# Kernel optimization log

Hardware: AMD Instinct MI355X
Metric: run time of the kernel (lower is better)

The kernel has to match this reference:

```python
import jax, jax.numpy as jnp
import numpy as np

N, E, D, ED, T, L = 10000, 160000, 128, 64, 4, 3
FIN, FOUT = D, D // T  # divide_input=False -> F_in = hidden; F_out = hidden // towers


def _w(key, *shape):
    return jax.random.normal(key, shape, dtype=jnp.float32) * 0.05


def setup_inputs() -> dict:
    key = jax.random.key(0)
    ks = iter(jax.random.split(key, 64))
    inp = {
        "x": jax.random.normal(next(ks), (N, D), jnp.float32),
        "edge_index": jax.random.randint(next(ks), (2, E), 0, N, jnp.int32),
        "edge_attr": jax.random.normal(next(ks), (E, ED), jnp.float32),
        # per-layer PNAConv params (stacked over L layers, T towers)
        "enc_W": _w(next(ks), L, ED, FIN), "enc_b": _w(next(ks), L, FIN),
        "pre_W1": _w(next(ks), L, T, 3 * FIN, FIN), "pre_b1": _w(next(ks), L, T, FIN),
        "pre_W2": _w(next(ks), L, T, FIN, FIN), "pre_b2": _w(next(ks), L, T, FIN),
        "post_W1": _w(next(ks), L, T, 4 * FIN, FOUT), "post_b1": _w(next(ks), L, T, FOUT),
        "post_W2": _w(next(ks), L, T, FOUT, FOUT), "post_b2": _w(next(ks), L, T, FOUT),
        "lin_W": _w(next(ks), L, D, D), "lin_b": _w(next(ks), L, D),
        # GRU (gate order r, z, n as in torch)
        "gru_Wi": _w(next(ks), D, 3 * D), "gru_Wh": _w(next(ks), D, 3 * D),
        "gru_bi": _w(next(ks), 3 * D), "gru_bh": _w(next(ks), 3 * D),
        # edge-update MLPs (shared across layers, as in the module)
        "fcu_W1": _w(next(ks), D, 2 * D), "fcu_b1": _w(next(ks), 2 * D),
        "fcu_W2": _w(next(ks), 2 * D, 2 * D), "fcu_b2": _w(next(ks), 2 * D),
        "fcv_W1": _w(next(ks), D, 2 * D), "fcv_b1": _w(next(ks), 2 * D),
        "fcv_W2": _w(next(ks), 2 * D, 2 * D), "fcv_b2": _w(next(ks), 2 * D),
        "fc_W1": _w(next(ks), 2 * D, 2 * D), "fc_b1": _w(next(ks), 2 * D),
        "fc_W2": _w(next(ks), 2 * D, ED), "fc_b2": _w(next(ks), ED),
        "eu_W1": _w(next(ks), 2 * ED, 2 * ED), "eu_b1": _w(next(ks), 2 * ED),
        "eu_W2": _w(next(ks), 2 * ED, ED), "eu_b2": _w(next(ks), ED),
    }
    return inp


def _pna_conv(x, src, dst, edge_attr, enc_W, enc_b, pW1, pb1, pW2, pb2,
              qW1, qb1, qW2, qb2, lW, lb):
    # message: pre-MLP on cat(x_i, x_j, enc(edge_attr)); split first Linear to avoid cat.
    e = edge_attr @ enc_W + enc_b                              # [E, FIN]
    Wi, Wj, We = pW1[:, :FIN], pW1[:, FIN:2 * FIN], pW1[:, 2 * FIN:]
    h = (jnp.einsum('ef,tfo->eto', x[dst], Wi)
         + jnp.einsum('ef,tfo->eto', x[src], Wj)
         + jnp.einsum('ef,tfo->eto', e, We) + pb1)             # [E, T, FIN]
    msg = jnp.einsum('etf,tfo->eto', jax.nn.relu(h), pW2) + pb2  # [E, T, FIN]
    # aggregate at target nodes (dst): mean / max / std
    cnt = jnp.maximum(jax.ops.segment_sum(jnp.ones((E,), msg.dtype), dst, N), 1.0)[:, None, None]
    mean = jax.ops.segment_sum(msg, dst, N) / cnt
    mean_sq = jax.ops.segment_sum(msg * msg, dst, N) / cnt
    std = jnp.sqrt(jax.nn.relu(mean_sq - mean * mean) + 1e-5)
    mx = jax.ops.segment_max(msg, dst, N)
    mx = jnp.where(jnp.isfinite(mx), mx, 0.0)
    xt = jnp.broadcast_to(x[:, None, :], (N, T, FIN))
    out = jnp.concatenate([xt, mean, mx, std], axis=-1)        # [N, T, 4*FIN]
    out = jax.nn.relu(jnp.einsum('ntf,tfo->nto', out, qW1) + qb1)
    out = jnp.einsum('ntf,tfo->nto', out, qW2) + qb2           # [N, T, FOUT]
    return out.reshape(N, D) @ lW + lb


def _gru(m, h, Wi, Wh, bi, bh):
    gi = m @ Wi + bi
    gh = h @ Wh + bh
    ir, iz, inn = jnp.split(gi, 3, axis=-1)
    hr, hz, hn = jnp.split(gh, 3, axis=-1)
    r = jax.nn.sigmoid(ir + hr)
    z = jax.nn.sigmoid(iz + hz)
    n = jnp.tanh(inn + r * hn)
    return (1.0 - z) * n + z * h


def _forward(x, edge_index, edge_attr,
             enc_W, enc_b, pre_W1, pre_b1, pre_W2, pre_b2,
             post_W1, post_b1, post_W2, post_b2, lin_W, lin_b,
             gru_Wi, gru_Wh, gru_bi, gru_bh,
             fcu_W1, fcu_b1, fcu_W2, fcu_b2,
             fcv_W1, fcv_b1, fcv_W2, fcv_b2,
             fc_W1, fc_b1, fc_W2, fc_b2,
             eu_W1, eu_b1, eu_W2, eu_b2):
    src, dst = edge_index[0], edge_index[1]
    out, h = x, x
    for i in range(L):
        m = _pna_conv(out, src, dst, edge_attr,
                      enc_W[i], enc_b[i], pre_W1[i], pre_b1[i], pre_W2[i], pre_b2[i],
                      post_W1[i], post_b1[i], post_W2[i], post_b2[i], lin_W[i], lin_b[i])
        h = _gru(m, h, gru_Wi, gru_Wh, gru_bi, gru_bh)
        out = h
        u, v = out[src], out[dst]
        fu = jax.nn.relu(jax.nn.relu(u @ fcu_W1 + fcu_b1) @ fcu_W2 + fcu_b2)
        fv = jax.nn.relu(jax.nn.relu(v @ fcv_W1 + fcv_b1) @ fcv_W2 + fcv_b2)
        m_ed = jax.nn.relu(jax.nn.relu(fu * fv @ fc_W1 + fc_b1) @ fc_W2 + fc_b2)
        edge_attr = jax.nn.relu(jnp.concatenate([m_ed, edge_attr], axis=1) @ eu_W1 + eu_b1) @ eu_W2 + eu_b2
    return out, edge_attr


def reference(x, edge_index, edge_attr,
              enc_W, enc_b, pre_W1, pre_b1, pre_W2, pre_b2,
              post_W1, post_b1, post_W2, post_b2, lin_W, lin_b,
              gru_Wi, gru_Wh, gru_bi, gru_bh,
              fcu_W1, fcu_b1, fcu_W2, fcu_b2,
              fcv_W1, fcv_b1, fcv_W2, fcv_b2,
              fc_W1, fc_b1, fc_W2, fc_b2,
              eu_W1, eu_b1, eu_W2, eu_b2):
    out, ea = _forward(x, edge_index, edge_attr,
                       enc_W, enc_b, pre_W1, pre_b1, pre_W2, pre_b2,
                       post_W1, post_b1, post_W2, post_b2, lin_W, lin_b,
                       gru_Wi, gru_Wh, gru_bi, gru_bh,
                       fcu_W1, fcu_b1, fcu_W2, fcu_b2,
                       fcv_W1, fcv_b1, fcv_W2, fcv_b2,
                       fc_W1, fc_b1, fc_W2, fc_b2,
                       eu_W1, eu_b1, eu_W2, eu_b2)
    return (out, ea, out)
```

## Files before the change

### kernel.cpp

```cpp
#include <hip/hip_runtime.h>
#include <hip/hip_bf16.h>
#include <math.h>

#define GN 10000
#define GNP 10112
#define GE 160000
#define GT 4
#define GL 3

typedef __attribute__((ext_vector_type(8))) short short8;
typedef __attribute__((ext_vector_type(4))) float f32x4;
typedef unsigned short u16;
typedef unsigned int u32;

__device__ __forceinline__ u16 f2b(float f) {
  unsigned u = __float_as_uint(f);
  unsigned r = (u + 0x7FFFu + ((u >> 16) & 1u)) >> 16;
  return (u16)r;
}
__device__ __forceinline__ float b2f(u16 b) {
  return __uint_as_float(((unsigned)b) << 16);
}

__device__ __forceinline__ void gl_lds16(const void* g, void* l) {
  __builtin_amdgcn_global_load_lds(
      (const __attribute__((address_space(1))) void*)g,
      (__attribute__((address_space(3))) void*)l, 16, 0, 0);
}

__device__ __forceinline__ int xcd_swz(int orig, int nwg) {
  int q = nwg >> 3, r = nwg & 7;
  int xcd = orig & 7, idx = orig >> 3;
  return (xcd < r ? xcd * (q + 1) : r * (q + 1) + (xcd - r) * q) + idx;
}

__global__ __launch_bounds__(256) void gemmz_k(
    const float* __restrict__ A0, const float* __restrict__ B0,
    const float* __restrict__ bias0, u16* __restrict__ Cv,
    int M, int N, int K, int lda, int ldb, int ldc,
    size_t aZ, size_t btZ, size_t bZ, int cCol)
{
  __shared__ float As[16][65];
  __shared__ float Bs[16][65];
  const int z = blockIdx.z;
  const float* A = A0 + (size_t)z * aZ;
  const float* B = B0 + (size_t)z * btZ;
  const float* bias = bias0 + (size_t)z * bZ;
  const int tid = threadIdx.x;
  const int brow = blockIdx.y * 64;
  const int tr = ((tid >> 4) & 15) << 2;
  const int tc = (tid & 15) << 2;
  float acc[4][4] = {{0.f}};

  for (int k0 = 0; k0 < K; k0 += 16) {
    for (int i = tid; i < 64 * 16; i += 256) {
      int r = i >> 4, c = i & 15;
      int gr = brow + r, gk = k0 + c;
      float v = 0.f;
      if (gr < M && gk < K) v = A[(size_t)gr * lda + gk];
      As[c][r] = v;
    }
    for (int i = tid; i < 16 * 64; i += 256) {
      int r = i >> 6, c = i & 63;
      int gk = k0 + r;
      Bs[r][c] = (gk < K && c < N) ? B[(size_t)gk * ldb + c] : 0.f;
    }
    __syncthreads();
#pragma unroll
    for (int kk = 0; kk < 16; ++kk) {
      float a[4], b[4];
#pragma unroll
      for (int i = 0; i < 4; ++i) a[i] = As[kk][tr + i];
#pragma unroll
      for (int j = 0; j < 4; ++j) b[j] = Bs[kk][tc + j];
#pragma unroll
      for (int i = 0; i < 4; ++i)
#pragma unroll
        for (int j = 0; j < 4; ++j) acc[i][j] += a[i] * b[j];
    }
    __syncthreads();
  }

#pragma unroll
  for (int i = 0; i < 4; ++i) {
    int gr = brow + tr + i;
    if (gr >= M) continue;
#pragma unroll
    for (int j = 0; j < 4; ++j) {
      int gc = tc + j;
      if (gc >= N) continue;
      Cv[(size_t)gr * ldc + z * cCol + gc] = f2b(acc[i][j] + bias[gc]);
    }
  }
}

template<bool RELU, bool OUTB, bool EAFILL>
__global__ __launch_bounds__(256) void mgemm_k(
    const u16* __restrict__ A,
    const u16* __restrict__ Bt, const float* __restrict__ bias,
    void* __restrict__ Cv,
    int M, int N, int K, int lda, int ldc,
    const float* __restrict__ ea, long e0)
{
  __shared__ u16 As[64 * 64];
  __shared__ u16 Bs[64 * 64];
  const int tid = threadIdx.x;
  const int brow = blockIdx.y * 64, bcol = blockIdx.x * 64;
  const int wid = tid >> 6, lane = tid & 63;
  const int wr = wid >> 1, wc = wid & 1;
  const int lrow = lane & 15, lk8 = (lane >> 4) * 8;

  f32x4 acc[2][2] = {};

  for (int k0 = 0; k0 < K; k0 += 64) {
#pragma unroll
    for (int s = 0; s < 2; ++s) {
      int c = tid + s * 256;
      int r = c >> 3, kq = (c & 7) * 8;
      const u16* sp = A + (size_t)(brow + r) * lda + k0 + kq;
      short8 v = *(const short8*)sp;
      int byt = (r * 128 + kq * 2) ^ ((r & 7) << 4);
      *(short8*)((char*)As + byt) = v;
    }
#pragma unroll
    for (int s = 0; s < 2; ++s) {
      int c = tid + s * 256;
      int r = c >> 3, kq = (c & 7) * 8;
      const u16* sp = Bt + (size_t)(bcol + r) * K + k0 + kq;
      short8 v = *(const short8*)sp;
      int byt = (r * 128 + kq * 2) ^ ((r & 7) << 4);
      *(short8*)((char*)Bs + byt) = v;
    }
    __syncthreads();
#pragma unroll
    for (int ks = 0; ks < 2; ++ks) {
      short8 a[2], b[2];
#pragma unroll
      for (int m = 0; m < 2; ++m) {
        int r = wr * 32 + m * 16 + lrow;
        int kk = ks * 32 + lk8;
        int byt = (r * 128 + kk * 2) ^ ((r & 7) << 4);
        a[m] = *(const short8*)((const char*)As + byt);
      }
#pragma unroll
      for (int n = 0; n < 2; ++n) {
        int r = wc * 32 + n * 16 + lrow;
        int kk = ks * 32 + lk8;
        int byt = (r * 128 + kk * 2) ^ ((r & 7) << 4);
        b[n] = *(const short8*)((const char*)Bs + byt);
      }
#pragma unroll
      for (int m = 0; m < 2; ++m)
#pragma unroll
        for (int n = 0; n < 2; ++n)
          acc[m][n] = __builtin_amdgcn_mfma_f32_16x16x32_bf16(a[m], b[n], acc[m][n], 0, 0, 0);
    }
    __syncthreads();
  }

#pragma unroll
  for (int m = 0; m < 2; ++m)
#pragma unroll
    for (int n = 0; n < 2; ++n) {
      int col = bcol + wc * 32 + n * 16 + (lane & 15);
      float bv = bias[col];
#pragma unroll
      for (int j = 0; j < 4; ++j) {
        int row = brow + wr * 32 + m * 16 + (lane >> 4) * 4 + j;
        float v = acc[m][n][j] + bv;
        if (RELU) v = fmaxf(v, 0.f);
        if (OUTB) ((u16*)Cv)[(size_t)row * ldc + col] = f2b(v);
        else      ((float*)Cv)[(size_t)row * ldc + col] = v;
      }
    }
  if (EAFILL) {
    for (int i = tid; i < 64 * 64; i += 256) {
      int r = i >> 6, c = i & 63;
      ((u16*)Cv)[(size_t)(brow + r) * 128 + 64 + c] =
          f2b(ea[(size_t)(e0 + brow + r) * 64 + c]);
    }
  }
}

template<bool RELU, bool OUTB>
__global__ __launch_bounds__(256) void mgemm_z_k(
    const u16* __restrict__ A0,
    const u16* __restrict__ Bt0, const float* __restrict__ bias0,
    void* __restrict__ Cv,
    int M, int N, int K, int lda, int ldc,
    size_t aZ, size_t btZ, size_t bZ, size_t cZ)
{
  __shared__ u16 As[64 * 64];
  __shared__ u16 Bs[64 * 64];
  const int z = blockIdx.z;
  const u16* A = A0 + (size_t)z * aZ;
  const u16* Bt = Bt0 + (size_t)z * btZ;
  const float* bias = bias0 + (size_t)z * bZ;
  const int tid = threadIdx.x;
  const int brow = blockIdx.y * 64, bcol = blockIdx.x * 64;
  const int wid = tid >> 6, lane = tid & 63;
  const int wr = wid >> 1, wc = wid & 1;
  const int lrow = lane & 15, lk8 = (lane >> 4) * 8;

  f32x4 acc[2][2] = {};

  for (int k0 = 0; k0 < K; k0 += 64) {
#pragma unroll
    for (int s = 0; s < 2; ++s) {
      int c = tid + s * 256;
      int r = c >> 3, kq = (c & 7) * 8;
      const u16* sp = A + (size_t)(brow + r) * lda + k0 + kq;
      short8 v = *(const short8*)sp;
      int byt = (r * 128 + kq * 2) ^ ((r & 7) << 4);
      *(short8*)((char*)As + byt) = v;
    }
#pragma unroll
    for (int s = 0; s < 2; ++s) {
      int c = tid + s * 256;
      int r = c >> 3, kq = (c & 7) * 8;
      const u16* sp = Bt + (size_t)(bcol + r) * K + k0 + kq;
      short8 v = *(const short8*)sp;
      int byt = (r * 128 + kq * 2) ^ ((r & 7) << 4);
      *(short8*)((char*)Bs + byt) = v;
    }
    __syncthreads();
#pragma unroll
    for (int ks = 0; ks < 2; ++ks) {
      short8 a[2], b[2];
#pragma unroll
      for (int m = 0; m < 2; ++m) {
        int r = wr * 32 + m * 16 + lrow;
        int kk = ks * 32 + lk8;
        int byt = (r * 128 + kk * 2) ^ ((r & 7) << 4);
        a[m] = *(const short8*)((const char*)As + byt);
      }
#pragma unroll
      for (int n = 0; n < 2; ++n) {
        int r = wc * 32 + n * 16 + lrow;
        int kk = ks * 32 + lk8;
        int byt = (r * 128 + kk * 2) ^ ((r & 7) << 4);
        b[n] = *(const short8*)((const char*)Bs + byt);
      }
#pragma unroll
      for (int m = 0; m < 2; ++m)
#pragma unroll
        for (int n = 0; n < 2; ++n)
          acc[m][n] = __builtin_amdgcn_mfma_f32_16x16x32_bf16(a[m], b[n], acc[m][n], 0, 0, 0);
    }
    __syncthreads();
  }

#pragma unroll
  for (int m = 0; m < 2; ++m)
#pragma unroll
    for (int n = 0; n < 2; ++n) {
      int col = bcol + wc * 32 + n * 16 + (lane & 15);
      float bv = bias[col];
#pragma unroll
      for (int j = 0; j < 4; ++j) {
        int row = brow + wr * 32 + m * 16 + (lane >> 4) * 4 + j;
        float v = acc[m][n][j] + bv;
        if (RELU) v = fmaxf(v, 0.f);
        if (OUTB) ((u16*)Cv + (size_t)z * cZ)[(size_t)row * ldc + col] = f2b(v);
        else      ((float*)Cv + (size_t)z * cZ)[(size_t)row * ldc + col] = v;
      }
    }
}

template<bool RELU, bool GATHER, bool MUL, bool OUTB>
__global__ __launch_bounds__(256) void mg2_k(
    const u16* __restrict__ A, const u16* __restrict__ A2,
    const int* __restrict__ idx, const int* __restrict__ idx2,
    const u16* __restrict__ Bt, const float* __restrict__ bias,
    void* __restrict__ Cv,
    int M, int N, int K, int lda, int ldc)
{
  __shared__ u16 As[128 * 64];
  __shared__ u16 Bs[128 * 64];
  __shared__ int ridx[128];
  __shared__ int ridx2[128];
  const int tid = threadIdx.x;
  const int brow = blockIdx.y * 128, bcol = blockIdx.x * 128;
  const int wid = tid >> 6, lane = tid & 63;
  const int wr = wid >> 1, wc = wid & 1;
  const int lrow = lane & 15, lkg = lane >> 4;

  if (GATHER) {
    if (tid < 128) {
      ridx[tid] = idx[brow + tid];
      if (MUL) ridx2[tid] = idx2[brow + tid];
    }
    __syncthreads();
  }

  f32x4 acc[4][4] = {};

  const char* srcA[4];
  const char* srcB[4];
#pragma unroll
  for (int s = 0; s < 4; ++s) {
    int i = tid + s * 256;
    int r = i >> 3, g = i & 7;
    size_t grow = GATHER ? (size_t)ridx[r] : (size_t)(brow + r);
    int gq = (g ^ (r & 7)) * 8;
    srcA[s] = (const char*)(A + grow * lda + gq);
    srcB[s] = (const char*)(Bt + (size_t)(bcol + r) * K + gq);
  }

  for (int k0 = 0; k0 < K; k0 += 64) {
    if constexpr (!MUL) {
#pragma unroll
      for (int s = 0; s < 4; ++s)
        gl_lds16(srcA[s] + (size_t)k0 * 2, (char*)As + s * 4096 + wid * 1024);
#pragma unroll
      for (int s = 0; s < 4; ++s)
        gl_lds16(srcB[s] + (size_t)k0 * 2, (char*)Bs + s * 4096 + wid * 1024);
    } else {
#pragma unroll
      for (int s = 0; s < 4; ++s) {
        int i = tid + s * 256;
        int r = i >> 3, kq = (i & 7) * 8;
        size_t grow = GATHER ? (size_t)ridx[r] : (size_t)(brow + r);
        size_t grow2 = GATHER ? (size_t)ridx2[r] : (size_t)(brow + r);
        const u16* sp = A + grow * lda + k0 + kq;
        short8 v = *(const short8*)sp;
        const u16* sp2 = A2 + grow2 * lda + k0 + kq;
        short8 v2 = *(const short8*)sp2;
#pragma unroll
        for (int e = 0; e < 8; ++e)
          v[e] = (short)f2b(b2f((u16)v[e]) * b2f((u16)v2[e]));
        int byt = (r * 128 + kq * 2) ^ ((r & 7) << 4);
        *(short8*)((char*)As + byt) = v;
      }
#pragma unroll
      for (int s = 0; s < 4; ++s) {
        int i = tid + s * 256;
        int r = i >> 3, kq = (i & 7) * 8;
        const u16* sp = Bt + (size_t)(bcol + r) * K + k0 + kq;
        short8 v = *(const short8*)sp;
        int byt = (r * 128 + kq * 2) ^ ((r & 7) << 4);
        *(short8*)((char*)Bs + byt) = v;
      }
    }
    __syncthreads();
#pragma unroll
    for (int ks = 0; ks < 2; ++ks) {
      const int kb = ks * 64 + lkg * 16;
      short8 a[4], b[4];
#pragma unroll
      for (int m = 0; m < 4; ++m) {
        int r = wr * 64 + m * 16 + lrow;
        int byt = (r * 128 + kb) ^ ((r & 7) << 4);
        a[m] = *(const short8*)((const char*)As + byt);
      }
#pragma unroll
      for (int n = 0; n < 4; ++n) {
        int r = wc * 64 + n * 16 + lrow;
        int byt = (r * 128 + kb) ^ ((r & 7) << 4);
        b[n] = *(const short8*)((const char*)Bs + byt);
      }
#pragma unroll
      for (int m = 0; m < 4; ++m)
#pragma unroll
        for (int n = 0; n < 4; ++n)
          acc[m][n] = __builtin_amdgcn_mfma_f32_16x16x32_bf16(a[m], b[n], acc[m][n], 0, 0, 0);
    }
    __syncthreads();
  }

#pragma unroll
  for (int m = 0; m < 4; ++m)
#pragma unroll
    for (int n = 0; n < 4; ++n) {
      int col = bcol + wc * 64 + n * 16 + lrow;
      float bv = bias[col];
#pragma unroll
      for (int j = 0; j < 4; ++j) {
        int row = brow + wr * 64 + m * 16 + lkg * 4 + j;
        float v = acc[m][n][j] + bv;
        if (RELU) v = fmaxf(v, 0.f);
        if (OUTB) ((u16*)Cv)[(size_t)row * ldc + col] = f2b(v);
        else      ((float*)Cv)[(size_t)row * ldc + col] = v;
      }
    }
}

__global__ __launch_bounds__(256) void convf_k(
    const u16* __restrict__ eab, const int* __restrict__ eidx,
    const int* __restrict__ src, const int* __restrict__ dst, long base,
    const u16* __restrict__ EWt, const float* __restrict__ bc,
    const u16* __restrict__ XIJ,
    const u16* __restrict__ W2t, const float* __restrict__ b2,
    float* __restrict__ sumb, float* __restrict__ sumsqb,
    unsigned* __restrict__ mxb, int Nn)
{
  __shared__ u16 AB[128 * 128];
  __shared__ u16 H[128 * 128];
  __shared__ int nid[128], sidm[128];
  u16* As = AB;
  u16* Bs = AB + 128 * 64;
  const int tid = threadIdx.x;
  const int brow = xcd_swz(blockIdx.x, gridDim.x) * 128;
  const int t = blockIdx.y;
  const int wid = tid >> 6, lane = tid & 63;
  const int wr = wid >> 1, wc = wid & 1;
  const int lrow = lane & 15, lkg = lane >> 4;

  __shared__ int eids[128];
  if (tid < 128) {
    int e = eidx[base + brow + tid];
    eids[tid] = e;
    nid[tid] = dst[e];
    sidm[tid] = src[e];
  }
  __syncthreads();

#pragma unroll
  for (int s = 0; s < 4; ++s) {
    int i = tid + s * 256;
    int r = i >> 3, g = i & 7;
    int gq = (g ^ (r & 7)) * 8;
    gl_lds16(eab + (size_t)eids[r] * 64 + gq, (char*)As + s * 4096 + wid * 1024);
  }
#pragma unroll
  for (int s = 0; s < 4; ++s) {
    int i = tid + s * 256;
    int r = i >> 3, g = i & 7;
    int gq = (g ^ (r & 7)) * 8;
    gl_lds16(EWt + (size_t)(t * 128 + r) * 64 + gq, (char*)Bs + s * 4096 + wid * 1024);
  }
  __syncthreads();

  f32x4 acc[4][4] = {};
#pragma unroll
  for (int ks = 0; ks < 2; ++ks) {
    const int kb = ks * 64 + lkg * 16;
    short8 a[4], b[4];
#pragma unroll
    for (int m = 0; m < 4; ++m) {
      int r = wr * 64 + m * 16 + lrow;
      int byt = (r * 128 + kb) ^ ((r & 7) << 4);
      a[m] = *(const short8*)((const char*)As + byt);
    }
#pragma unroll
    for (int n = 0; n < 4; ++n) {
      int r = wc * 64 + n * 16 + lrow;
      int byt = (r * 128 + kb) ^ ((r & 7) << 4);
      b[n] = *(const short8*)((const char*)Bs + byt);
    }
#pragma unroll
    for (int m = 0; m < 4; ++m)
#pragma unroll
      for (int n = 0; n < 4; ++n)
        acc[m][n] = __builtin_amdgcn_mfma_f32_16x16x32_bf16(a[m], b[n], acc[m][n], 0, 0, 0);
  }

#pragma unroll
  for (int m = 0; m < 4; ++m)
#pragma unroll
    for (int n = 0; n < 4; ++n) {
      int cl = wc * 64 + n * 16 + lrow;
      float bv = bc[t * 128 + cl];
#pragma unroll
      for (int j = 0; j < 4; ++j) {
        int rl = wr * 64 + m * 16 + lkg * 4 + j;
        int byt = (rl * 256 + cl * 2) ^ ((rl & 7) << 4);
        *(u16*)((char*)H + byt) = f2b(acc[m][n][j] + bv);
      }
    }
  __syncthreads();

#pragma unroll
  for (int s = 0; s < 8; ++s) {
    int i = tid + s * 256;
    int r = i >> 4, g = i & 15;
    int gs = (g & 8) | ((g & 7) ^ (r & 7));
    gl_lds16(W2t + (size_t)t * 16384 + (size_t)r * 128 + gs * 8,
             (char*)AB + s * 4096 + wid * 1024);
  }

#pragma unroll
  for (int s = 0; s < 8; ++s) {
    int i = tid + s * 256;
    int row = i >> 4, q = i & 15;
    int byt = (row * 256 + q * 16) ^ ((row & 7) << 4);
    short8 h8 = *(const short8*)((const char*)H + byt);
    short8 a8 = *(const short8*)(XIJ + (size_t)nid[row] * 1024 + t * 128 + q * 8);
    short8 c8 = *(const short8*)(XIJ + (size_t)sidm[row] * 1024 + 512 + t * 128 + q * 8);
#pragma unroll
    for (int e = 0; e < 8; ++e) {
      float v = b2f((u16)h8[e]) + b2f((u16)a8[e]) + b2f((u16)c8[e]);
      h8[e] = (short)f2b(fmaxf(v, 0.f));
    }
    *(short8*)((char*)H + byt) = h8;
  }
  __syncthreads();

  f32x4 acc2[4][4] = {};
#pragma unroll
  for (int ks = 0; ks < 4; ++ks) {
    const int kb = ks * 64 + lkg * 16;
    short8 a[4], b[4];
#pragma unroll
    for (int m = 0; m < 4; ++m) {
      int r = wr * 64 + m * 16 + lrow;
      int byt = (r * 256 + kb) ^ ((r & 7) << 4);
      a[m] = *(const short8*)((const char*)H + byt);
    }
#pragma unroll
    for (int n = 0; n < 4; ++n) {
      int c = wc * 64 + n * 16 + lrow;
      int byt = (c * 256 + kb) ^ ((c & 7) << 4);
      b[n] = *(const short8*)((const char*)AB + byt);
    }
#pragma unroll
    for (int m = 0; m < 4; ++m)
#pragma unroll
      for (int n = 0; n < 4; ++n)
        acc2[m][n] = __builtin_amdgcn_mfma_f32_16x16x32_bf16(a[m], b[n], acc2[m][n], 0, 0, 0);
  }
  __syncthreads();

#pragma unroll
  for (int m = 0; m < 4; ++m)
#pragma unroll
    for (int n = 0; n < 4; ++n) {
      int col = wc * 64 + n * 16 + lrow;
      float bv = b2[t * 128 + col];
#pragma unroll
      for (int j = 0; j < 4; ++j) {
        int row = wr * 64 + m * 16 + lkg * 4 + j;
        int byt = (row * 256 + col * 2) ^ ((row & 7) << 4);
        *(u16*)((char*)H + byt) = f2b(acc2[m][n][j] + bv);
      }
    }
  __syncthreads();

  {
    const int col = tid & 127, half = tid >> 7;
    const int r0 = half * 64;
    float* sb = sumb + (size_t)t * Nn * 128;
    float* qb = sumsqb + (size_t)t * Nn * 128;
    unsigned* xbp = mxb + (size_t)t * Nn * 128;
    int cur = nid[r0];
    float sacc = 0.f, qacc = 0.f, mxv = -INFINITY;
    for (int rr = 0; rr < 64; ++rr) {
      int row = r0 + rr;
      int nd = nid[row];
      if (nd != cur) {
        size_t o = (size_t)cur * 128 + col;
        atomicAdd(&sb[o], sacc);
        atomicAdd(&qb[o], qacc);
        unsigned ub = __float_as_uint(mxv);
        atomicMax(&xbp[o], (ub & 0x80000000u) ? ~ub : (ub | 0x80000000u));
        cur = nd; sacc = 0.f; qacc = 0.f; mxv = -INFINITY;
      }
      int byt = (row * 256 + col * 2) ^ ((row & 7) << 4);
      float v = b2f(*(const u16*)((const char*)H + byt));
      sacc += v; qacc += v * v; mxv = fmaxf(mxv, v);
    }
    size_t o = (size_t)cur * 128 + col;
    atomicAdd(&sb[o], sacc);
    atomicAdd(&qb[o], qacc);
    unsigned ub = __float_as_uint(mxv);
    atomicMax(&xbp[o], (ub & 0x80000000u) ? ~ub : (ub | 0x80000000u));
  }
}

__global__ __launch_bounds__(256) void eu_fused_k(
    const u16* __restrict__ C3b,
    const u16* __restrict__ euW1t, const float* __restrict__ eu_b1,
    const u16* __restrict__ euW2t, const float* __restrict__ eu_b2,
    float* __restrict__ EAp, u16* __restrict__ eab, long e0)
{
  __shared__ u16 SM[128 * 128];
  __shared__ u16 W2s[64 * 128];
  u16* As = SM;
  u16* Bs = SM + 128 * 64;
  const int tid = threadIdx.x;
  const int brow = blockIdx.x * 128;
  const int wid = tid >> 6, lane = tid & 63;
  const int wr = wid >> 1, wc = wid & 1;
  const int lrow = lane & 15, lkg = lane >> 4;

#pragma unroll
  for (int s = 0; s < 4; ++s) {
    int i = tid + s * 256;
    int r = i >> 4, g = i & 15;
    int gs = (g & 8) | ((g & 7) ^ (r & 7));
    gl_lds16(euW2t + (size_t)r * 128 + gs * 8, (char*)W2s + s * 4096 + wid * 1024);
  }

  const char* srcA[4];
  const char* srcB[4];
#pragma unroll
  for (int s = 0; s < 4; ++s) {
    int i = tid + s * 256;
    int r = i >> 3, g = i & 7;
    int gq = (g ^ (r & 7)) * 8;
    srcA[s] = (const char*)(C3b + (size_t)(brow + r) * 128 + gq);
    srcB[s] = (const char*)(euW1t + (size_t)r * 128 + gq);
  }

  f32x4 acc[4][4] = {};
  for (int k0 = 0; k0 < 128; k0 += 64) {
#pragma unroll
    for (int s = 0; s < 4; ++s)
      gl_lds16(srcA[s] + (size_t)k0 * 2, (char*)As + s * 4096 + wid * 1024);
#pragma unroll
    for (int s = 0; s < 4; ++s)
      gl_lds16(srcB[s] + (size_t)k0 * 2, (char*)Bs + s * 4096 + wid * 1024);
    __syncthreads();
#pragma unroll
    for (int ks = 0; ks < 2; ++ks) {
      const int kb = ks * 64 + lkg * 16;
      short8 a[4], b[4];
#pragma unroll
      for (int m = 0; m < 4; ++m) {
        int r = wr * 64 + m * 16 + lrow;
        int byt = (r * 128 + kb) ^ ((r & 7) << 4);
        a[m] = *(const short8*)((const char*)As + byt);
      }
#pragma unroll
      for (int n = 0; n < 4; ++n) {
        int r = wc * 64 + n * 16 + lrow;
        int byt = (r * 128 + kb) ^ ((r & 7) << 4);
        b[n] = *(const short8*)((const char*)Bs + byt);
      }
#pragma unroll
      for (int m = 0; m < 4; ++m)
#pragma unroll
        for (int n = 0; n < 4; ++n)
          acc[m][n] = __builtin_amdgcn_mfma_f32_16x16x32_bf16(a[m], b[n], acc[m][n], 0, 0, 0);
    }
    __syncthreads();
  }

#pragma unroll
  for (int m = 0; m < 4; ++m)
#pragma unroll
    for (int n = 0; n < 4; ++n) {
      int col = wc * 64 + n * 16 + lrow;
      float bv = eu_b1[col];
#pragma unroll
      for (int j = 0; j < 4; ++j) {
        int row = wr * 64 + m * 16 + lkg * 4 + j;
        float v = fmaxf(acc[m][n][j] + bv, 0.f);
        int byt = (row * 256 + col * 2) ^ ((row & 7) << 4);
        *(u16*)((char*)SM + byt) = f2b(v);
      }
    }
  __syncthreads();

  f32x4 acc2[2][4] = {};
#pragma unroll
  for (int ks = 0; ks < 4; ++ks) {
    const int kb = ks * 64 + lkg * 16;
    short8 a[2], b[4];
#pragma unroll
    for (int m = 0; m < 2; ++m) {
      int r = wid * 32 + m * 16 + lrow;
      int byt = (r * 256 + kb) ^ ((r & 7) << 4);
      a[m] = *(const short8*)((const char*)SM + byt);
    }
#pragma unroll
    for (int n = 0; n < 4; ++n) {
      int c = n * 16 + lrow;
      int byt = (c * 256 + kb) ^ ((c & 7) << 4);
      b[n] = *(const short8*)((const char*)W2s + byt);
    }
#pragma unroll
    for (int m = 0; m < 2; ++m)
#pragma unroll
      for (int n = 0; n < 4; ++n)
        acc2[m][n] = __builtin_amdgcn_mfma_f32_16x16x32_bf16(a[m], b[n], acc2[m][n], 0, 0, 0);
  }

#pragma unroll
  for (int m = 0; m < 2; ++m)
#pragma unroll
    for (int n = 0; n < 4; ++n) {
      int col = n * 16 + lrow;
      float bv = eu_b2[col];
#pragma unroll
      for (int j = 0; j < 4; ++j) {
        int row = wid * 32 + m * 16 + lkg * 4 + j;
        float v = acc2[m][n][j] + bv;
        size_t o = (size_t)(e0 + brow + row) * 64 + col;
        EAp[o] = v;
        eab[o] = f2b(v);
      }
    }
}

__global__ void deg_kernel(const int* __restrict__ dst, int* __restrict__ deg, int E)
{
  int e = blockIdx.x * blockDim.x + threadIdx.x;
  if (e < E) atomicAdd(&deg[dst[e]], 1);
}

__global__ void scan_kernel(const int* __restrict__ deg, int* __restrict__ rowptr, int n)
{
  __shared__ int wsum[4];
  __shared__ int carry_s;
  const int tid = threadIdx.x, lane = tid & 63, wv = tid >> 6;
  if (tid == 0) carry_s = 0;
  __syncthreads();
  for (int base = 0; base < n; base += 256) {
    int i = base + tid;
    int v = (i < n) ? deg[i] : 0;
    int s = v;
#pragma unroll
    for (int off = 1; off < 64; off <<= 1) {
      int t = __shfl_up(s, off, 64);
      if (lane >= off) s += t;
    }
    if (lane == 63) wsum[wv] = s;
    __syncthreads();
    int wo = carry_s;
    for (int q = 0; q < wv; ++q) wo += wsum[q];
    int tot = carry_s + wsum[0] + wsum[1] + wsum[2] + wsum[3];
    __syncthreads();
    if (i < n) rowptr[i] = wo + s - v;
    if (tid == 0) carry_s = tot;
    __syncthreads();
  }
  if (threadIdx.x == 0) rowptr[n] = carry_s;
}

__global__ void scatter_kernel(const int* __restrict__ dst, int* __restrict__ cursor,
                               int* __restrict__ eidx, int E)
{
  int e = blockIdx.x * blockDim.x + threadIdx.x;
  if (e < E) {
    int p = atomicAdd(&cursor[dst[e]], 1);
    eidx[p] = e;
  }
}

__global__ void wtb_kernel(const float* __restrict__ W, u16* __restrict__ Wt,
                           int K, int N, size_t wtStride)
{
  int b = blockIdx.y;
  const float* Wb = W + (size_t)b * K * N;
  u16* Wtb = Wt + (size_t)b * wtStride;
  for (int i = blockIdx.x * blockDim.x + threadIdx.x; i < K * N;
       i += gridDim.x * blockDim.x) {
    int k = i / N, n = i % N;
    Wtb[(size_t)n * K + k] = f2b(Wb[i]);
  }
}

__global__ void wtbsub_kernel(const float* __restrict__ W, u16* __restrict__ Wt,
                              int k0, size_t lStride)
{
  int b = blockIdx.y;
  int l = b >> 2, t = b & 3;
  const float* Wb = W + (size_t)b * 384 * 128 + (size_t)k0 * 128;
  u16* Wtb = Wt + (size_t)l * lStride + (size_t)t * 16384;
  for (int i = blockIdx.x * blockDim.x + threadIdx.x; i < 16384;
       i += gridDim.x * blockDim.x) {
    int n = i >> 7, k = i & 127;
    Wtb[(size_t)n * 128 + k] = f2b(Wb[(size_t)k * 128 + n]);
  }
}

__global__ void ewcomb_kernel(const float* __restrict__ encW,
                              const float* __restrict__ preW1, u16* __restrict__ EWt)
{
  int i = blockIdx.x * blockDim.x + threadIdx.x;
  if (i >= GL * 512 * 64) return;
  int l = i / (512 * 64);
  int rem = i % (512 * 64);
  int n = rem / 64, k = rem % 64;
  int t = n >> 7, o = n & 127;
  const float* eW = encW + (size_t)l * 64 * 128 + (size_t)k * 128;
  const float* pW = preW1 + ((size_t)(l * GT + t) * 384 + 256) * 128 + o;
  float s = 0.f;
  for (int j = 0; j < 128; ++j) s += eW[j] * pW[(size_t)j * 128];
  EWt[i] = f2b(s);
}

__global__ void bcomb_kernel(const float* __restrict__ encb,
                             const float* __restrict__ preb1,
                             const float* __restrict__ preW1, float* __restrict__ bc)
{
  int i = blockIdx.x * blockDim.x + threadIdx.x;
  if (i >= GL * 512) return;
  int l = i / 512, n = i % 512;
  int t = n >> 7, o = n & 127;
  const float* eb = encb + (size_t)l * 128;
  const float* pW = preW1 + ((size_t)(l * GT + t) * 384 + 256) * 128 + o;
  float s = preb1[(size_t)(l * GT + t) * 128 + o];
  for (int j = 0; j < 128; ++j) s += eb[j] * pW[(size_t)j * 128];
  bc[i] = s;
}

__global__ void biaspad_kernel(const float* __restrict__ b32, float* __restrict__ b64, int total)
{
  int i = blockIdx.x * blockDim.x + threadIdx.x;
  if (i >= total) return;
  b64[(i / 32) * 64 + (i % 32)] = b32[i];
}

__global__ void f2b_kernel(const float* __restrict__ in, u16* __restrict__ out, int n)
{
  int i = blockIdx.x * blockDim.x + threadIdx.x;
  if (i < n) out[i] = f2b(in[i]);
}

__global__ void agg_init_kernel(float* __restrict__ s, float* __restrict__ ss,
                                unsigned* __restrict__ mx, int total)
{
  int i = blockIdx.x * blockDim.x + threadIdx.x;
  if (i >= total) return;
  s[i] = 0.f; ss[i] = 0.f; mx[i] = 0x007FFFFFu;
}

__global__ void finalize_kernel(
    const float* __restrict__ sumb, const float* __restrict__ sumsqb,
    const unsigned* __restrict__ mxb, const int* __restrict__ rowptr,
    const float* __restrict__ x, u16* __restrict__ catb4, int Nn)
{
  int i = blockIdx.x * blockDim.x + threadIdx.x;
  if (i >= 4 * Nn * 128) return;
  int t = i / (Nn * 128);
  int j = i - t * Nn * 128;
  int n = j >> 7, c = j & 127;
  float cnt = fmaxf((float)(rowptr[n + 1] - rowptr[n]), 1.f);
  float mean = sumb[i] / cnt;
  float msq  = sumsqb[i] / cnt;
  float sd = sqrtf(fmaxf(msq - mean * mean, 0.f) + 1e-5f);
  unsigned u = mxb[i];
  unsigned bits = (u & 0x80000000u) ? (u & 0x7FFFFFFFu) : ~u;
  float mxv = __uint_as_float(bits);
  if ((bits & 0x7F800000u) == 0x7F800000u) mxv = 0.f;
  u16* cb = catb4 + ((size_t)t * GNP + n) * 512;
  cb[c]       = f2b(x[(size_t)n * 128 + c]);
  cb[128 + c] = f2b(mean);
  cb[256 + c] = f2b(mxv);
  cb[384 + c] = f2b(sd);
}

__global__ void gru_kernel(const float* __restrict__ gi, const float* __restrict__ gh,
                           const float* __restrict__ h, float* __restrict__ hout,
                           u16* __restrict__ xbo, int total)
{
  int i = blockIdx.x * blockDim.x + threadIdx.x;
  if (i >= total) return;
  int n = i >> 7, c = i & 127;
  const float* gin = gi + (size_t)n * 384;
  const float* ghn = gh + (size_t)n * 384;
  float ir = gin[c], iz = gin[128 + c], inn = gin[256 + c];
  float hr = ghn[c], hz = ghn[128 + c], hn = ghn[256 + c];
  float r = 1.f / (1.f + __expf(-(ir + hr)));
  float z = 1.f / (1.f + __expf(-(iz + hz)));
  float nn = tanhf(inn + r * hn);
  float v = (1.f - z) * nn + z * h[i];
  hout[i] = v;
  xbo[i] = f2b(v);
}

extern "C" void kernel_launch(void* const* d_in, const int* in_sizes, int n_in,
                              void* d_out, int out_size, void* d_ws, size_t ws_size,
                              hipStream_t stream)
{
  const int N_ = GN, E_ = GE, Np = GNP;

  const float* x_in   = (const float*)d_in[0];
  const int*   src    = (const int*)d_in[1];
  const int*   dst    = src + E_;
  const float* ea_in  = (const float*)d_in[2];
  const float* enc_W  = (const float*)d_in[3];
  const float* enc_b  = (const float*)d_in[4];
  const float* pre_W1 = (const float*)d_in[5];
  const float* pre_b1 = (const float*)d_in[6];
  const float* pre_W2 = (const float*)d_in[7];
  const float* pre_b2 = (const float*)d_in[8];
  const float* post_W1 = (const float*)d_in[9];
  const float* post_b1 = (const float*)d_in[10];
  const float* post_W2 = (const float*)d_in[11];
  const float* post_b2 = (const float*)d_in[12];
  const float* lin_W  = (const float*)d_in[13];
  const float* lin_b  = (const float*)d_in[14];
  const float* gru_Wi = (const float*)d_in[15];
  const float* gru_Wh = (const float*)d_in[16];
  const float* gru_bi = (const float*)d_in[17];
  const float* gru_bh = (const float*)d_in[18];
  const float* fcu_W1 = (const float*)d_in[19];
  const float* fcu_b1 = (const float*)d_in[20];
  const float* fcu_W2 = (const float*)d_in[21];
  const float* fcu_b2 = (const float*)d_in[22];
  const float* fcv_W1 = (const float*)d_in[23];
  const float* fcv_b1 = (const float*)d_in[24];
  const float* fcv_W2 = (const float*)d_in[25];
  const float* fcv_b2 = (const float*)d_in[26];
  const float* fc_W1  = (const float*)d_in[27];
  const float* fc_b1  = (const float*)d_in[28];
  const float* fc_W2  = (const float*)d_in[29];
  const float* fc_b2  = (const float*)d_in[30];
  const float* eu_W1  = (const float*)d_in[31];
  const float* eu_b1  = (const float*)d_in[32];
  const float* eu_W2  = (const float*)d_in[33];
  const float* eu_b2  = (const float*)d_in[34];

  size_t used = 0;
  char* w = (char*)d_ws;
  auto alloc = [&](size_t bytes) {
    char* p = w + used;
    used += (bytes + 255) & ~(size_t)255;
    return p;
  };
  float*    sumb   = (float*)alloc((size_t)N_ * 512 * 4);
  float*    sumsqb = (float*)alloc((size_t)N_ * 512 * 4);
  unsigned* mxb    = (unsigned*)alloc((size_t)N_ * 512 * 4);
  float*    q1   = (float*)alloc((size_t)Np * 256 * 4);
  u16*      q2b  = (u16*)alloc((size_t)Np * 128 * 2);
  u16*      mbb  = (u16*)alloc((size_t)Np * 128 * 2);
  float*    gib  = (float*)alloc((size_t)Np * 384 * 4);
  float*    ghb  = (float*)alloc((size_t)Np * 384 * 4);
  float*    Hb   = (float*)alloc((size_t)N_ * 128 * 4);
  u16*      xb   = (u16*)alloc((size_t)Np * 128 * 2);
  u16*      catb4 = (u16*)alloc((size_t)4 * Np * 512 * 2);
  u16*      eab  = (u16*)alloc((size_t)E_ * 64 * 2);
  u16*      XIJ  = (u16*)alloc((size_t)Np * 1024 * 2);
  u16*      FUV1b = (u16*)alloc((size_t)Np * 512 * 2);
  u16*      FUVb  = (u16*)alloc((size_t)Np * 512 * 2);
  float*    zb   = (float*)alloc(1024 * 4);
  u16* WIJt   = (u16*)alloc((size_t)GL * 1024 * 128 * 2);
  u16* EWt    = (u16*)alloc((size_t)GL * 512 * 64 * 2);
  float* bcomb = (float*)alloc((size_t)GL * 512 * 4);
  u16* preW2t = (u16*)alloc((size_t)GL * GT * 128 * 128 * 2);
  u16* postW1t = (u16*)alloc((size_t)GL * GT * 64 * 512 * 2);
  float* postb1p = (float*)alloc((size_t)GL * GT * 64 * 4);
  u16* linWt  = (u16*)alloc((size_t)GL * 128 * 128 * 2);
  u16* gruWit = (u16*)alloc((size_t)384 * 128 * 2);
  u16* gruWht = (u16*)alloc((size_t)384 * 128 * 2);
  u16* fuvW1t = (u16*)alloc((size_t)512 * 128 * 2);
  u16* fcuW2t = (u16*)alloc((size_t)256 * 256 * 2);
  u16* fcvW2t = (u16*)alloc((size_t)256 * 256 * 2);
  float* fuvb1 = (float*)alloc(512 * 4);
  float* fuvb2 = (float*)alloc(512 * 4);
  u16* fcW1t  = (u16*)alloc((size_t)256 * 256 * 2);
  u16* fcW2t  = (u16*)alloc((size_t)64 * 256 * 2);
  u16* euW1t  = (u16*)alloc((size_t)128 * 128 * 2);
  u16* euW2t  = (u16*)alloc((size_t)64 * 128 * 2);
  int* eidx   = (int*)alloc((size_t)E_ * 4);
  int* degb   = (int*)alloc((size_t)(N_ + 1) * 4);
  int* rowptr = (int*)alloc((size_t)(N_ + 1) * 4);
  int* cursor = (int*)alloc((size_t)(N_ + 1) * 4);

  size_t avail = (ws_size > used + 4096) ? (ws_size - used - 4096) : 0;
  long Ec = (long)(avail / 768);
  if (Ec > E_) Ec = E_;
  Ec &= ~255L;
  if (Ec < 256) return;
  char* arena = alloc((size_t)Ec * 768);
  if (used > ws_size) return;
  const int nchunks = (int)((E_ + Ec - 1) / Ec);
  u16* C1b = (u16*)arena;
  u16* C3b = (u16*)(arena + (size_t)Ec * 512);

  float* out = (float*)d_out;
  float* EAp = out + (size_t)N_ * 128;

  hipMemsetAsync(degb, 0, (size_t)N_ * 4, stream);
  deg_kernel<<<(E_ + 255) / 256, 256, 0, stream>>>(dst, degb, E_);
  scan_kernel<<<1, 256, 0, stream>>>(degb, rowptr, N_);
  hipMemcpyAsync(cursor, rowptr, (size_t)N_ * 4, hipMemcpyDeviceToDevice, stream);
  scatter_kernel<<<(E_ + 255) / 256, 256, 0, stream>>>(dst, cursor, eidx, E_);

  hipMemsetAsync(postW1t, 0, (size_t)GL * GT * 64 * 512 * 2, stream);
  hipMemsetAsync(postb1p, 0, (size_t)GL * GT * 64 * 4, stream);
  hipMemsetAsync(zb, 0, 1024 * 4, stream);
  {
    dim3 gb(48, GL);
    wtb_kernel<<<gb, 256, 0, stream>>>(lin_W, linWt, 128, 128, 128 * 128);
    dim3 gt(48, GL * GT);
    wtb_kernel<<<gt, 256, 0, stream>>>(pre_W2, preW2t, 128, 128, 128 * 128);
    wtb_kernel<<<gt, 256, 0, stream>>>(post_W1, postW1t, 512, 32, 64 * 512);
    dim3 gs(16, GL * GT);
    wtbsub_kernel<<<gs, 256, 0, stream>>>(pre_W1, WIJt, 0, 131072);
    wtbsub_kernel<<<gs, 256, 0, stream>>>(pre_W1, WIJt + 65536, 128, 131072);
    ewcomb_kernel<<<(GL * 512 * 64 + 255) / 256, 256, 0, stream>>>(enc_W, pre_W1, EWt);
    bcomb_kernel<<<(GL * 512 + 255) / 256, 256, 0, stream>>>(enc_b, pre_b1, pre_W1, bcomb);
    dim3 g1(48, 1);
    wtb_kernel<<<g1, 256, 0, stream>>>(gru_Wi, gruWit, 128, 384, 384 * 128);
    wtb_kernel<<<g1, 256, 0, stream>>>(gru_Wh, gruWht, 128, 384, 384 * 128);
    wtb_kernel<<<g1, 256, 0, stream>>>(fcu_W1, fuvW1t, 128, 256, 0);
    wtb_kernel<<<g1, 256, 0, stream>>>(fcv_W1, fuvW1t + 256 * 128, 128, 256, 0);
    wtb_kernel<<<g1, 256, 0, stream>>>(fcu_W2, fcuW2t, 256, 256, 0);
    wtb_kernel<<<g1, 256, 0, stream>>>(fcv_W2, fcvW2t, 256, 256, 0);
    wtb_kernel<<<g1, 256, 0, stream>>>(fc_W1, fcW1t, 256, 256, 0);
    wtb_kernel<<<g1, 256, 0, stream>>>(fc_W2, fcW2t, 256, 64, 0);
    wtb_kernel<<<g1, 256, 0, stream>>>(eu_W1, euW1t, 128, 128, 0);
    wtb_kernel<<<g1, 256, 0, stream>>>(eu_W2, euW2t, 128, 64, 0);
  }
  biaspad_kernel<<<(GL * GT * 32 + 255) / 256, 256, 0, stream>>>(
      post_b1, postb1p, GL * GT * 32);
  hipMemcpyAsync(fuvb1, fcu_b1, 256 * 4, hipMemcpyDeviceToDevice, stream);
  hipMemcpyAsync(fuvb1 + 256, fcv_b1, 256 * 4, hipMemcpyDeviceToDevice, stream);
  hipMemcpyAsync(fuvb2, fcu_b2, 256 * 4, hipMemcpyDeviceToDevice, stream);
  hipMemcpyAsync(fuvb2 + 256, fcv_b2, 256 * 4, hipMemcpyDeviceToDevice, stream);

  f2b_kernel<<<(N_ * 128 + 255) / 256, 256, 0, stream>>>(x_in, xb, N_ * 128);
  f2b_kernel<<<(E_ * 64 + 255) / 256, 256, 0, stream>>>(ea_in, eab, E_ * 64);

  const float* x_cur = x_in;
  const float* ea_cur = ea_in;

  for (int l = 0; l < GL; ++l) {
    agg_init_kernel<<<(N_ * 512 + 255) / 256, 256, 0, stream>>>(sumb, sumsqb, mxb, N_ * 512);
    {
      dim3 gX(8, Np / 128);
      mg2_k<false, false, false, true><<<gX, 256, 0, stream>>>(
          xb, nullptr, nullptr, nullptr, WIJt + (size_t)l * 131072, zb,
          XIJ, Np, 1024, 128, 128, 1024);
    }
    {
      dim3 gC(E_ / 128, GT);
      convf_k<<<gC, 256, 0, stream>>>(
          eab, eidx, src, dst, 0,
          EWt + (size_t)l * 512 * 64, bcomb + (size_t)l * 512, XIJ,
          preW2t + (size_t)l * GT * 16384, pre_b2 + (size_t)l * 512,
          sumb, sumsqb, mxb, N_);
    }
    finalize_kernel<<<(4 * N_ * 128 + 255) / 256, 256, 0, stream>>>(
        sumb, sumsqb, mxb, rowptr, x_cur, catb4, N_);
    {
      dim3 gP1(1, Np / 64, 4);
      mgemm_z_k<true, false><<<gP1, 256, 0, stream>>>(
          catb4, postW1t + (size_t)l * GT * 64 * 512, postb1p + (size_t)l * GT * 64,
          q1, Np, 64, 512, 512, 64,
          (size_t)Np * 512, (size_t)64 * 512, 64, (size_t)Np * 64);
      dim3 gP2(1, (N_ + 63) / 64, 4);
      gemmz_k<<<gP2, 256, 0, stream>>>(
          q1, post_W2 + (size_t)l * GT * 32 * 32, post_b2 + (size_t)l * GT * 32,
          q2b, N_, 32, 32, 64, 32, 128,
          (size_t)Np * 64, (size_t)32 * 32, 32, 32);
    }
    {
      dim3 gL(1, Np / 128), gG(3, Np / 128);
      mg2_k<false, false, false, true><<<gL, 256, 0, stream>>>(
          q2b, nullptr, nullptr, nullptr, linWt + (size_t)l * 128 * 128,
          lin_b + (size_t)l * 128, mbb, Np, 128, 128, 128, 128);
      mg2_k<false, false, false, false><<<gG, 256, 0, stream>>>(
          mbb, nullptr, nullptr, nullptr, gruWit, gru_bi, gib, Np, 384, 128, 128, 384);
      mg2_k<false, false, false, false><<<gG, 256, 0, stream>>>(
          xb, nullptr, nullptr, nullptr, gruWht, gru_bh, ghb, Np, 384, 128, 128, 384);
    }
    gru_kernel<<<(N_ * 128 + 255) / 256, 256, 0, stream>>>(
        gib, ghb, x_cur, Hb, xb, N_ * 128);

    {
      dim3 gF1(4, Np / 128);
      mg2_k<true, false, false, true><<<gF1, 256, 0, stream>>>(
          xb, nullptr, nullptr, nullptr, fuvW1t, fuvb1, FUV1b, Np, 512, 128, 128, 512);
      dim3 gF2(4, Np / 64, 2);
      mgemm_z_k<true, true><<<gF2, 256, 0, stream>>>(
          FUV1b, fcuW2t, fuvb2, FUVb, Np, 256, 256, 512, 256,
          (size_t)256, (size_t)256 * 256, 256, (size_t)Np * 256);
    }
    const u16* FUb = FUVb;
    const u16* FVb = FUVb + (size_t)Np * 256;
    for (int c = 0; c < nchunks; ++c) {
      long e0 = (long)c * Ec;
      int Mc = (int)(((long)E_ - e0 < Ec) ? ((long)E_ - e0) : Ec);
      dim3 g2m(2, Mc / 128), g64(1, Mc / 64);
      mg2_k<true, true, true, true><<<g2m, 256, 0, stream>>>(
          FUb, FVb, src + e0, dst + e0, fcW1t, fc_b1, C1b, Mc, 256, 256, 256, 256);
      mgemm_k<true, true, true><<<g64, 256, 0, stream>>>(
          C1b, fcW2t, fc_b2, C3b, Mc, 64, 256, 256, 128, ea_cur, e0);
      eu_fused_k<<<Mc / 128, 256, 0, stream>>>(
          C3b, euW1t, eu_b1, euW2t, eu_b2, EAp, eab, e0);
    }

    x_cur = Hb;
    ea_cur = EAp;
  }

  hipMemcpyAsync(out, x_cur, (size_t)N_ * 128 * 4, hipMemcpyDeviceToDevice, stream);
  hipMemcpyAsync(out + (size_t)N_ * 128 + (size_t)E_ * 64, x_cur,
                 (size_t)N_ * 128 * 4, hipMemcpyDeviceToDevice, stream);
}
```

Measured before the change: 1.490 ms.

## Loop towers inside convf kernel to reuse gathered edge-attribute fragments

The conv kernel previously launched one block per (edge tile, tower), so each of the four towers re-gathered the same 128 edge-attribute rows and the edge index metadata. Now one block handles all towers in a loop: the gathered edge rows are loaded once into registers as MFMA A-fragments and reused for every tower's encoder GEMM. This removes redundant random gathers but cuts the grid by four, which reduces parallelism and latency hiding, and adds register pressure from holding the A fragments across the loop.

```diff
diff --git a/kernel.cpp b/kernel.cpp
--- a/kernel.cpp
+++ b/kernel.cpp
@@ -387,7 +387,7 @@
 
 __global__ __launch_bounds__(256) void convf_k(
     const u16* __restrict__ eab, const int* __restrict__ eidx,
-    const int* __restrict__ src, const int* __restrict__ dst, long base,
+    const int* __restrict__ src, const int* __restrict__ dst,
     const u16* __restrict__ EWt, const float* __restrict__ bc,
     const u16* __restrict__ XIJ,
     const u16* __restrict__ W2t, const float* __restrict__ b2,
@@ -396,19 +396,16 @@
 {
   __shared__ u16 AB[128 * 128];
   __shared__ u16 H[128 * 128];
-  __shared__ int nid[128], sidm[128];
-  u16* As = AB;
-  u16* Bs = AB + 128 * 64;
+  __shared__ int nid[128], sidm[128], eids[128];
+  u16* Bs = AB;
   const int tid = threadIdx.x;
   const int brow = xcd_swz(blockIdx.x, gridDim.x) * 128;
-  const int t = blockIdx.y;
   const int wid = tid >> 6, lane = tid & 63;
   const int wr = wid >> 1, wc = wid & 1;
   const int lrow = lane & 15, lkg = lane >> 4;
 
-  __shared__ int eids[128];
   if (tid < 128) {
-    int e = eidx[base + brow + tid];
+    int e = eidx[brow + tid];
     eids[tid] = e;
     nid[tid] = dst[e];
     sidm[tid] = src[e];
@@ -420,150 +417,160 @@
     int i = tid + s * 256;
     int r = i >> 3, g = i & 7;
     int gq = (g ^ (r & 7)) * 8;
-    gl_lds16(eab + (size_t)eids[r] * 64 + gq, (char*)As + s * 4096 + wid * 1024);
-  }
-#pragma unroll
-  for (int s = 0; s < 4; ++s) {
-    int i = tid + s * 256;
-    int r = i >> 3, g = i & 7;
-    int gq = (g ^ (r & 7)) * 8;
-    gl_lds16(EWt + (size_t)(t * 128 + r) * 64 + gq, (char*)Bs + s * 4096 + wid * 1024);
+    gl_lds16(eab + (size_t)eids[r] * 64 + gq, (char*)H + s * 4096 + wid * 1024);
   }
   __syncthreads();
 
-  f32x4 acc[4][4] = {};
+  short8 aA[2][4];
 #pragma unroll
   for (int ks = 0; ks < 2; ++ks) {
     const int kb = ks * 64 + lkg * 16;
-    short8 a[4], b[4];
 #pragma unroll
     for (int m = 0; m < 4; ++m) {
       int r = wr * 64 + m * 16 + lrow;
       int byt = (r * 128 + kb) ^ ((r & 7) << 4);
-      a[m] = *(const short8*)((const char*)As + byt);
-    }
-#pragma unroll
-    for (int n = 0; n < 4; ++n) {
-      int r = wc * 64 + n * 16 + lrow;
-      int byt = (r * 128 + kb) ^ ((r & 7) << 4);
-      b[n] = *(const short8*)((const char*)Bs + byt);
-    }
+      aA[ks][m] = *(const short8*)((const char*)H + byt);
+    }
+  }
+
+  for (int t = 0; t < GT; ++t) {
+#pragma unroll
+    for (int s = 0; s < 4; ++s) {
+      int i = tid + s * 256;
+      int r = i >> 3, g = i & 7;
+      int gq = (g ^ (r & 7)) * 8;
+      gl_lds16(EWt + (size_t)(t * 128 + r) * 64 + gq, (char*)Bs + s * 4096 + wid * 1024);
+    }
+    __syncthreads();
+
+    f32x4 acc[4][4] = {};
+#pragma unroll
+    for (int ks = 0; ks < 2; ++ks) {
+      const int kb = ks * 64 + lkg * 16;
+      short8 b[4];
+#pragma unroll
+      for (int n = 0; n < 4; ++n) {
+        int r = wc * 64 + n * 16 + lrow;
+        int byt = (r * 128 + kb) ^ ((r & 7) << 4);
+        b[n] = *(const short8*)((const char*)Bs + byt);
+      }
+#pragma unroll
+      for (int m = 0; m < 4; ++m)
+#pragma unroll
+        for (int n = 0; n < 4; ++n)
+          acc[m][n] = __builtin_amdgcn_mfma_f32_16x16x32_bf16(aA[ks][m], b[n], acc[m][n], 0, 0, 0);
+    }
+
 #pragma unroll
     for (int m = 0; m < 4; ++m)
 #pragma unroll
-      for (int n = 0; n < 4; ++n)
-        acc[m][n] = __builtin_amdgcn_mfma_f32_16x16x32_bf16(a[m], b[n], acc[m][n], 0, 0, 0);
-  }
-
-#pragma unroll
-  for (int m = 0; m < 4; ++m)
-#pragma unroll
-    for (int n = 0; n < 4; ++n) {
-      int cl = wc * 64 + n * 16 + lrow;
-      float bv = bc[t * 128 + cl];
-#pragma unroll
-      for (int j = 0; j < 4; ++j) {
-        int rl = wr * 64 + m * 16 + lkg * 4 + j;
-        int byt = (rl * 256 + cl * 2) ^ ((rl & 7) << 4);
-        *(u16*)((char*)H + byt) = f2b(acc[m][n][j] + bv);
-      }
-    }
-  __syncthreads();
-
-#pragma unroll
-  for (int s = 0; s < 8; ++s) {
-    int i = tid + s * 256;
-    int r = i >> 4, g = i & 15;
-    int gs = (g & 8) | ((g & 7) ^ (r & 7));
-    gl_lds16(W2t + (size_t)t * 16384 + (size_t)r * 128 + gs * 8,
-             (char*)AB + s * 4096 + wid * 1024);
-  }
-
-#pragma unroll
-  for (int s = 0; s < 8; ++s) {
-    int i = tid + s * 256;
-    int row = i >> 4, q = i & 15;
-    int byt = (row * 256 + q * 16) ^ ((row & 7) << 4);
-    short8 h8 = *(const short8*)((const char*)H + byt);
-    short8 a8 = *(const short8*)(XIJ + (size_t)nid[row] * 1024 + t * 128 + q * 8);
-    short8 c8 = *(const short8*)(XIJ + (size_t)sidm[row] * 1024 + 512 + t * 128 + q * 8);
-#pragma unroll
-    for (int e = 0; e < 8; ++e) {
-      float v = b2f((u16)h8[e]) + b2f((u16)a8[e]) + b2f((u16)c8[e]);
-      h8[e] = (short)f2b(fmaxf(v, 0.f));
-    }
-    *(short8*)((char*)H + byt) = h8;
-  }
-  __syncthreads();
-
-  f32x4 acc2[4][4] = {};
-#pragma unroll
-  for (int ks = 0; ks < 4; ++ks) {
-    const int kb = ks * 64 + lkg * 16;
-    short8 a[4], b[4];
-#pragma unroll
-    for (int m = 0; m < 4; ++m) {
-      int r = wr * 64 + m * 16 + lrow;
-      int byt = (r * 256 + kb) ^ ((r & 7) << 4);
-      a[m] = *(const short8*)((const char*)H + byt);
-    }
-#pragma unroll
-    for (int n = 0; n < 4; ++n) {
-      int c = wc * 64 + n * 16 + lrow;
-      int byt = (c * 256 + kb) ^ ((c & 7) << 4);
-      b[n] = *(const short8*)((const char*)AB + byt);
-    }
+      for (int n = 0; n < 4; ++n) {
+        int cl = wc * 64 + n * 16 + lrow;
+        float bv = bc[t * 128 + cl];
+#pragma unroll
+        for (int j = 0; j < 4; ++j) {
+          int rl = wr * 64 + m * 16 + lkg * 4 + j;
+          int byt = (rl * 256 + cl * 2) ^ ((rl & 7) << 4);
+          *(u16*)((char*)H + byt) = f2b(acc[m][n][j] + bv);
+        }
+      }
+    __syncthreads();
+
+#pragma unroll
+    for (int s = 0; s < 8; ++s) {
+      int i = tid + s * 256;
+      int r = i >> 4, g = i & 15;
+      int gs = (g & 8) | ((g & 7) ^ (r & 7));
+      gl_lds16(W2t + (size_t)t * 16384 + (size_t)r * 128 + gs * 8,
+               (char*)AB + s * 4096 + wid * 1024);
+    }
+
+#pragma unroll
+    for (int s = 0; s < 8; ++s) {
+      int i = tid + s * 256;
+      int row = i >> 4, q = i & 15;
+      int byt = (row * 256 + q * 16) ^ ((row & 7) << 4);
+      short8 h8 = *(const short8*)((const char*)H + byt);
+      short8 a8 = *(const short8*)(XIJ + (size_t)nid[row] * 1024 + t * 128 + q * 8);
+      short8 c8 = *(const short8*)(XIJ + (size_t)sidm[row] * 1024 + 512 + t * 128 + q * 8);
+#pragma unroll
+      for (int e = 0; e < 8; ++e) {
+        float v = b2f((u16)h8[e]) + b2f((u16)a8[e]) + b2f((u16)c8[e]);
+        h8[e] = (short)f2b(fmaxf(v, 0.f));
+      }
+      *(short8*)((char*)H + byt) = h8;
+    }
+    __syncthreads();
+
+    f32x4 acc2[4][4] = {};
+#pragma unroll
+    for (int ks = 0; ks < 4; ++ks) {
+      const int kb = ks * 64 + lkg * 16;
+      short8 a[4], b[4];
+#pragma unroll
+      for (int m = 0; m < 4; ++m) {
+        int r = wr * 64 + m * 16 + lrow;
+        int byt = (r * 256 + kb) ^ ((r & 7) << 4);
+        a[m] = *(const short8*)((const char*)H + byt);
+      }
+#pragma unroll
+      for (int n = 0; n < 4; ++n) {
+        int c = wc * 64 + n * 16 + lrow;
+        int byt = (c * 256 + kb) ^ ((c & 7) << 4);
+        b[n] = *(const short8*)((const char*)AB + byt);
+      }
+#pragma unroll
+      for (int m = 0; m < 4; ++m)
+#pragma unroll
+        for (int n = 0; n < 4; ++n)
+          acc2[m][n] = __builtin_amdgcn_mfma_f32_16x16x32_bf16(a[m], b[n], acc2[m][n], 0, 0, 0);
+    }
+    __syncthreads();
+
 #pragma unroll
     for (int m = 0; m < 4; ++m)
 #pragma unroll
-      for (int n = 0; n < 4; ++n)
-        acc2[m][n] = __builtin_amdgcn_mfma_f32_16x16x32_bf16(a[m], b[n], acc2[m][n], 0, 0, 0);
-  }
-  __syncthreads();
-
-#pragma unroll
-  for (int m = 0; m < 4; ++m)
-#pragma unroll
-    for (int n = 0; n < 4; ++n) {
-      int col = wc * 64 + n * 16 + lrow;
-      float bv = b2[t * 128 + col];
-#pragma unroll
-      for (int j = 0; j < 4; ++j) {
-        int row = wr * 64 + m * 16 + lkg * 4 + j;
+      for (int n = 0; n < 4; ++n) {
+        int col = wc * 64 + n * 16 + lrow;
+        float bv = b2[t * 128 + col];
+#pragma unroll
+        for (int j = 0; j < 4; ++j) {
+          int row = wr * 64 + m * 16 + lkg * 4 + j;
+          int byt = (row * 256 + col * 2) ^ ((row & 7) << 4);
+          *(u16*)((char*)H + byt) = f2b(acc2[m][n][j] + bv);
+        }
+      }
+    __syncthreads();
+
+    {
+      const int col = tid & 127, half = tid >> 7;
+      const int r0 = half * 64;
+      float* sb = sumb + (size_t)t * Nn * 128;
+      float* qb = sumsqb + (size_t)t * Nn * 128;
+      unsigned* xbp = mxb + (size_t)t * Nn * 128;
+      int cur = nid[r0];
+      float sacc = 0.f, qacc = 0.f, mxv = -INFINITY;
+      for (int rr = 0; rr < 64; ++rr) {
+        int row = r0 + rr;
+        int nd = nid[row];
+        if (nd != cur) {
+          size_t o = (size_t)cur * 128 + col;
+          atomicAdd(&sb[o], sacc);
+          atomicAdd(&qb[o], qacc);
+          unsigned ub = __float_as_uint(mxv);
+          atomicMax(&xbp[o], (ub & 0x80000000u) ? ~ub : (ub | 0x80000000u));
+          cur = nd; sacc = 0.f; qacc = 0.f; mxv = -INFINITY;
+        }
         int byt = (row * 256 + col * 2) ^ ((row & 7) << 4);
-        *(u16*)((char*)H + byt) = f2b(acc2[m][n][j] + bv);
-      }
-    }
-  __syncthreads();
-
-  {
-    const int col = tid & 127, half = tid >> 7;
-    const int r0 = half * 64;
-    float* sb = sumb + (size_t)t * Nn * 128;
-    float* qb = sumsqb + (size_t)t * Nn * 128;
-    unsigned* xbp = mxb + (size_t)t * Nn * 128;
-    int cur = nid[r0];
-    float sacc = 0.f, qacc = 0.f, mxv = -INFINITY;
-    for (int rr = 0; rr < 64; ++rr) {
-      int row = r0 + rr;
-      int nd = nid[row];
-      if (nd != cur) {
-        size_t o = (size_t)cur * 128 + col;
-        atomicAdd(&sb[o], sacc);
-        atomicAdd(&qb[o], qacc);
-        unsigned ub = __float_as_uint(mxv);
-        atomicMax(&xbp[o], (ub & 0x80000000u) ? ~ub : (ub | 0x80000000u));
-        cur = nd; sacc = 0.f; qacc = 0.f; mxv = -INFINITY;
-      }
-      int byt = (row * 256 + col * 2) ^ ((row & 7) << 4);
-      float v = b2f(*(const u16*)((const char*)H + byt));
-      sacc += v; qacc += v * v; mxv = fmaxf(mxv, v);
-    }
-    size_t o = (size_t)cur * 128 + col;
-    atomicAdd(&sb[o], sacc);
-    atomicAdd(&qb[o], qacc);
-    unsigned ub = __float_as_uint(mxv);
-    atomicMax(&xbp[o], (ub & 0x80000000u) ? ~ub : (ub | 0x80000000u));
+        float v = b2f(*(const u16*)((const char*)H + byt));
+        sacc += v; qacc += v * v; mxv = fmaxf(mxv, v);
+      }
+      size_t o = (size_t)cur * 128 + col;
+      atomicAdd(&sb[o], sacc);
+      atomicAdd(&qb[o], qacc);
+      unsigned ub = __float_as_uint(mxv);
+      atomicMax(&xbp[o], (ub & 0x80000000u) ? ~ub : (ub | 0x80000000u));
+    }
   }
 }
 
@@ -1017,14 +1024,11 @@
           xb, nullptr, nullptr, nullptr, WIJt + (size_t)l * 131072, zb,
           XIJ, Np, 1024, 128, 128, 1024);
     }
-    {
-      dim3 gC(E_ / 128, GT);
-      convf_k<<<gC, 256, 0, stream>>>(
-          eab, eidx, src, dst, 0,
-          EWt + (size_t)l * 512 * 64, bcomb + (size_t)l * 512, XIJ,
-          preW2t + (size_t)l * GT * 16384, pre_b2 + (size_t)l * 512,
-          sumb, sumsqb, mxb, N_);
-    }
+    convf_k<<<E_ / 128, 256, 0, stream>>>(
+        eab, eidx, src, dst,
+        EWt + (size_t)l * 512 * 64, bcomb + (size_t)l * 512, XIJ,
+        preW2t + (size_t)l * GT * 16384, pre_b2 + (size_t)l * 512,
+        sumb, sumsqb, mxb, N_);
     finalize_kernel<<<(4 * N_ * 128 + 255) / 256, 256, 0, stream>>>(
         sumb, sumsqb, mxb, rowptr, x_cur, catb4, N_);
     {
```

Result: slower. 1.830 ms (+22.9%).
